# Kernel tuning notes

Hardware: AMD Instinct MI355X
Metric: run time of the kernel (lower is better)

Reference implementation:

```python
import jax, jax.numpy as jnp
import numpy as np

N_NODES = 100000
N_EDGES = 1600000
MUL = 32            # channel multiplicity for every irrep
INV_SQRT_MUL = 1.0 / np.sqrt(32.0)
# path constants: wigner-3j norms (1/sqrt3 for 0x1->1 and 1x1->0, 1/sqrt6 for 1x1->1)
# combined with fan-in path normalization (fan=32 for 0e out, fan=64 for 1o out, 2 paths)
C_DOT = 1.0 / np.sqrt(3.0 * 32.0)
C_SCL = 1.0 / np.sqrt(3.0 * 64.0)
C_CRS = 1.0 / np.sqrt(6.0 * 64.0)


def setup_inputs() -> dict:
    key = jax.random.key(0)
    ks = jax.random.split(key, 12)
    x = jax.random.normal(ks[0], (N_NODES, 128), jnp.float32)
    pos = jax.random.normal(ks[1], (N_NODES, 3), jnp.float32)
    edge_index = jax.random.randint(ks[2], (2, N_EDGES), 0, N_NODES, jnp.int32)
    # o3.Linear(32x0e+32x1o -> 32x0e+32x0e+32x1o): per-irrep channel mixing
    W_node_s = jax.random.normal(ks[3], (32, 64), jnp.float32)   # 0e -> (scalars|gates)
    W_node_v = jax.random.normal(ks[4], (32, 32), jnp.float32)   # 1o -> 1o
    # FullyConnectedTensorProduct(32x0e+32x1o, 1x1o -> 32x0e+32x1o): 3 CG paths
    W_tp_d = jax.random.normal(ks[5], (32, 32), jnp.float32)     # 1o x 1o -> 0e (dot)
    W_tp_s = jax.random.normal(ks[6], (32, 32), jnp.float32)     # 0e x 1o -> 1o
    W_tp_c = jax.random.normal(ks[7], (32, 32), jnp.float32)     # 1o x 1o -> 1o (cross)
    # o3.Linear(32x0e+32x1o -> 32x0e+32x1o)
    W_msg_s = jax.random.normal(ks[8], (32, 32), jnp.float32)
    W_msg_v = jax.random.normal(ks[9], (32, 32), jnp.float32)
    ln_gamma = jnp.ones((128,), jnp.float32)
    ln_beta = jnp.zeros((128,), jnp.float32)
    return {"x": x, "pos": pos, "edge_index": edge_index,
            "W_node_s": W_node_s, "W_node_v": W_node_v,
            "W_tp_d": W_tp_d, "W_tp_s": W_tp_s, "W_tp_c": W_tp_c,
            "W_msg_s": W_msg_s, "W_msg_v": W_msg_v,
            "ln_gamma": ln_gamma, "ln_beta": ln_beta}


def reference(x, pos, edge_index, W_node_s, W_node_v, W_tp_d, W_tp_s, W_tp_c,
              W_msg_s, W_msg_v, ln_gamma, ln_beta):
    N = x.shape[0]
    row, col = edge_index[0], edge_index[1]
    # split node irreps: 32 scalars (0e) | 32 vectors (1o) of dim 3
    s = x[:, :32]                       # [N,32]
    v = x[:, 32:].reshape(-1, 32, 3)    # [N,32,3]
    # lin_node (equivariant linear, path-normalized by 1/sqrt(fan_in)=1/sqrt(32))
    h_s = (s @ W_node_s) * INV_SQRT_MUL                          # [N,64]
    h_v = jnp.einsum('nid,ij->njd', v, W_node_v) * INV_SQRT_MUL  # [N,32,3]
    # Gate: relu scalars, sigmoid gates multiply the gated vectors
    sc = jax.nn.relu(h_s[:, :32])                                # [N,32]
    hv = h_v * jax.nn.sigmoid(h_s[:, 32:])[:, :, None]           # [N,32,3]
    # spherical harmonics l=1, component norm: sqrt(3)*unit vec in e3nn (y,z,x) order
    rel = pos[col] - pos[row]                                    # [E,3]
    unit = rel / jnp.sqrt(jnp.sum(rel * rel, -1, keepdims=True) + 1e-12)
    u = jnp.sqrt(3.0) * unit[:, (1, 2, 0)]                       # [E,3]
    # gather source-node features per edge
    sj = sc[col]                                                 # [E,32]
    vj = hv[col]                                                 # [E,32,3]
    # CG tensor product paths
    dot = jnp.einsum('eid,ed->ei', vj, u)                        # 1o x 1o -> 0e
    crs = jnp.cross(vj, u[:, None, :])                           # 1o x 1o -> 1o
    m0 = (dot @ W_tp_d) * C_DOT                                  # [E,32]
    m1 = (sj @ W_tp_s)[:, :, None] * u[:, None, :] * C_SCL \
         + jnp.einsum('eid,ik->ekd', crs, W_tp_c) * C_CRS        # [E,32,3]
    m = jnp.concatenate([m0, m1.reshape(-1, 96)], -1)            # [E,128]
    # scatter-mean over destination nodes (row)
    deg = jax.ops.segment_sum(jnp.ones_like(row, jnp.float32), row,
                              num_segments=N).clip(1.0)
    mi = jax.ops.segment_sum(m, row, num_segments=N) / deg[:, None]
    # lin_msg
    ms = (mi[:, :32] @ W_msg_s) * INV_SQRT_MUL
    mv = jnp.einsum('nid,ij->njd', mi[:, 32:].reshape(-1, 32, 3),
                    W_msg_v) * INV_SQRT_MUL
    o = jnp.concatenate([ms, mv.reshape(-1, 96)], -1)            # [N,128]
    # LayerNorm over 128 dims (as in the original, affine)
    mu = o.mean(-1, keepdims=True)
    var = o.var(-1, keepdims=True)
    o = (o - mu) / jnp.sqrt(var + 1e-5) * ln_gamma + ln_beta
    return x + o
```

## Files before the change

### kernel.cpp

```cpp
#include <hip/hip_runtime.h>
#include <math.h>


static constexpr float INV_SQRT_MUL = 0.17677669529663687f;
static constexpr float C_DOT = 0.10206207261596575f;
static constexpr float C_SCL = 0.07216878364870322f;
static constexpr float C_CRS = 0.05103103630798288f;
static constexpr float SQRT3 = 1.7320508075688772f;
static constexpr int MAXDEG = 48;
static constexpr int FEAT_B = 2048;
static constexpr int SCAT_B = 2048;

#define WS_ALIGN(x) (((x) + 255) & ~(size_t)255)

__device__ __forceinline__ unsigned short f2bf(float v) {
    unsigned int b = __float_as_uint(v);
    b += 0x7FFFu + ((b >> 16) & 1u);
    return (unsigned short)(b >> 16);
}
__device__ __forceinline__ float bf2f(unsigned short u) {
    return __uint_as_float(((unsigned int)u) << 16);
}

__global__ __launch_bounds__(1024)
void fuse_zero(const float* __restrict__ Wtpd, const float* __restrict__ Wtps,
               const float* __restrict__ Wtpc, const float* __restrict__ Wms,
               const float* __restrict__ Wmv, float* __restrict__ Wall,
               int* __restrict__ cnt, int N) {
    int t = threadIdx.x;
    if (blockIdx.x == 0) {
        int i = t >> 5, j = t & 31;
        float a = 0.f, b = 0.f, c = 0.f;
#pragma unroll
        for (int k = 0; k < 32; ++k) {
            a += Wtpd[i * 32 + k] * Wms[k * 32 + j];
            b += Wtps[i * 32 + k] * Wmv[k * 32 + j];
            c += Wtpc[i * 32 + k] * Wmv[k * 32 + j];
        }
        Wall[t]        = a * (C_DOT * INV_SQRT_MUL);
        Wall[1024 + t] = b * (C_SCL * INV_SQRT_MUL);
        Wall[2048 + t] = c * (C_CRS * INV_SQRT_MUL);
    } else {
        int i = (blockIdx.x - 1) * 1024 + t;
        if (i < N) cnt[i] = 0;
    }
}

template <bool FAT>
__global__ __launch_bounds__(128)
void phase1(const float* __restrict__ x, const float* __restrict__ Wns,
            const float* __restrict__ Wnv, const float* __restrict__ pos,
            const int* __restrict__ eidx, unsigned short* __restrict__ feat,
            int* __restrict__ cnt, void* __restrict__ slots_raw, int N, int E) {
    int t = threadIdx.x;
    if (blockIdx.x < FEAT_B) {
        float w[32], wg[32];
        int d = 0, pidx;
        if (t < 32) {
            pidx = t * 4;
#pragma unroll
            for (int k = 0; k < 32; ++k) w[k] = Wns[k * 64 + t];
        } else {
            int cc = t - 32; d = cc >> 5; int i = cc & 31;
            pidx = i * 4 + 1 + d;
#pragma unroll
            for (int k = 0; k < 32; ++k) { w[k] = Wnv[k * 32 + i]; wg[k] = Wns[k * 64 + 32 + i]; }
        }
        __shared__ float xs[128];
        for (int n = blockIdx.x; n < N; n += FEAT_B) {
            xs[t] = x[(size_t)n * 128 + t];
            __syncthreads();
            float val;
            if (t < 32) {
                float h = 0.f;
#pragma unroll
                for (int k = 0; k < 32; ++k) h += xs[k] * w[k];
                val = fmaxf(h * INV_SQRT_MUL, 0.f);
            } else {
                float h = 0.f, g = 0.f;
#pragma unroll
                for (int k = 0; k < 32; ++k) { h += xs[32 + k * 3 + d] * w[k]; g += xs[k] * wg[k]; }
                float sig = 1.f / (1.f + expf(-g * INV_SQRT_MUL));
                val = h * INV_SQRT_MUL * sig;
            }
            feat[(size_t)n * 128 + pidx] = f2bf(val);
            __syncthreads();
        }
    } else {
        int tid = (blockIdx.x - FEAT_B) * 128 + t;
        int Q = E >> 2;
        const int4* r4p = (const int4*)eidx;
        const int4* c4p = (const int4*)(eidx + E);
        float4* slotsF = (float4*)slots_raw;
        int*    slotsI = (int*)slots_raw;
        for (int q = tid; q < Q; q += SCAT_B * 128) {
            int4 R = r4p[q];
            int4 C = c4p[q];
            int rr[4] = {R.x, R.y, R.z, R.w};
            int cc[4] = {C.x, C.y, C.z, C.w};
            if (FAT) {
                float prx[4], pry[4], prz[4], pcx[4], pcy[4], pcz[4];
#pragma unroll
                for (int k = 0; k < 4; ++k) {
                    prx[k] = pos[rr[k] * 3 + 0]; pry[k] = pos[rr[k] * 3 + 1]; prz[k] = pos[rr[k] * 3 + 2];
                    pcx[k] = pos[cc[k] * 3 + 0]; pcy[k] = pos[cc[k] * 3 + 1]; pcz[k] = pos[cc[k] * 3 + 2];
                }
#pragma unroll
                for (int k = 0; k < 4; ++k) {
                    float rx = pcx[k] - prx[k], ry = pcy[k] - pry[k], rz = pcz[k] - prz[k];
                    float inv = rsqrtf(rx * rx + ry * ry + rz * rz + 1e-12f) * SQRT3;
                    int p = atomicAdd(&cnt[rr[k]], 1);
                    if (p < MAXDEG)
                        slotsF[(size_t)rr[k] * MAXDEG + p] =
                            make_float4(ry * inv, rz * inv, rx * inv, __int_as_float(cc[k]));
                }
            } else {
#pragma unroll
                for (int k = 0; k < 4; ++k) {
                    int p = atomicAdd(&cnt[rr[k]], 1);
                    if (p < MAXDEG) slotsI[(size_t)rr[k] * MAXDEG + p] = cc[k];
                }
            }
        }
        for (int e = (Q << 2) + tid; e < E; e += SCAT_B * 128) {
            int r = eidx[e], c = eidx[E + e];
            int p = atomicAdd(&cnt[r], 1);
            if (p < MAXDEG) {
                if (FAT) {
                    float rx = pos[c * 3 + 0] - pos[r * 3 + 0];
                    float ry = pos[c * 3 + 1] - pos[r * 3 + 1];
                    float rz = pos[c * 3 + 2] - pos[r * 3 + 2];
                    float inv = rsqrtf(rx * rx + ry * ry + rz * rz + 1e-12f) * SQRT3;
                    slotsF[(size_t)r * MAXDEG + p] = make_float4(ry * inv, rz * inv, rx * inv, __int_as_float(c));
                } else {
                    slotsI[(size_t)r * MAXDEG + p] = c;
                }
            }
        }
    }
}

__global__ __launch_bounds__(256)
void agg_fat(const float* __restrict__ x, const ushort4* __restrict__ feat,
             const int* __restrict__ cnt, const float4* __restrict__ slots,
             const float* __restrict__ Wall, const float* __restrict__ gamma,
             const float* __restrict__ beta, float* __restrict__ out, int N) {
    int t = threadIdx.x;
    __shared__ float wlds[3072];
    __shared__ float4 finA[8][32];
    __shared__ float4 finB[8][32];
    {
        float4* w4 = (float4*)wlds;
        const float4* g4 = (const float4*)Wall;
        for (int i = t; i < 768; i += 256) w4[i] = g4[i];
    }
    int hw = t >> 5, lane = t & 31;
    int n = blockIdx.x * 8 + hw;
    bool live = (n < N);
    int deg = live ? cnt[n] : 0;
    int c = min(deg, MAXDEG);
    const float4* bucket = slots + (size_t)(live ? n : 0) * MAXDEG;

    float D = 0.f, S0 = 0.f, S1 = 0.f, S2 = 0.f, C0 = 0.f, C1 = 0.f, C2 = 0.f;
    auto body = [&](int j) {
        float4 q = bucket[j];
        int col = __float_as_int(q.w);
        ushort4 f = feat[(size_t)col * 32 + lane];
        float sj = bf2f(f.x);
        float h0 = bf2f(f.y), h1 = bf2f(f.z), h2 = bf2f(f.w);
        D  += h0 * q.x + h1 * q.y + h2 * q.z;
        S0 += sj * q.x; S1 += sj * q.y; S2 += sj * q.z;
        C0 += h1 * q.z - h2 * q.y;
        C1 += h2 * q.x - h0 * q.z;
        C2 += h0 * q.y - h1 * q.x;
    };
    int j = 0;
    for (; j + 3 < c; j += 4) { body(j); body(j + 1); body(j + 2); body(j + 3); }
    for (; j < c; ++j) body(j);

    finA[hw][lane] = make_float4(D, S0, S1, S2);
    finB[hw][lane] = make_float4(C0, C1, C2, 0.f);
    __syncthreads();

    float invdeg = 1.0f / (float)((deg > 0) ? deg : 1);
    float a0 = 0.f, aV0 = 0.f, aV1 = 0.f, aV2 = 0.f;
#pragma unroll 8
    for (int i = 0; i < 32; ++i) {
        float4 a = finA[hw][i];
        float4 b = finB[hw][i];
        float wd = wlds[i * 32 + lane];
        float ws = wlds[1024 + i * 32 + lane];
        float wc = wlds[2048 + i * 32 + lane];
        a0  += a.x * wd;
        aV0 += a.y * ws + b.x * wc;
        aV1 += a.z * ws + b.y * wc;
        aV2 += a.w * ws + b.z * wc;
    }
    float vd = a0 * invdeg;
    float v0 = aV0 * invdeg, v1 = aV1 * invdeg, v2 = aV2 * invdeg;

    float s1 = vd + v0 + v1 + v2;
    float s2 = vd * vd + v0 * v0 + v1 * v1 + v2 * v2;
#pragma unroll
    for (int m = 16; m >= 1; m >>= 1) {
        s1 += __shfl_xor(s1, m);
        s2 += __shfl_xor(s2, m);
    }
    float mu = s1 * (1.f / 128.f);
    float var = s2 * (1.f / 128.f) - mu * mu;
    float rstd = rsqrtf(var + 1e-5f);

    if (live) {
        size_t base = (size_t)n * 128;
        int chv = 32 + lane * 3;
        float xv0 = __builtin_nontemporal_load(&x[base + lane]);
        float xa  = __builtin_nontemporal_load(&x[base + chv + 0]);
        float xb  = __builtin_nontemporal_load(&x[base + chv + 1]);
        float xc  = __builtin_nontemporal_load(&x[base + chv + 2]);
        __builtin_nontemporal_store(xv0 + (vd - mu) * rstd * gamma[lane] + beta[lane], &out[base + lane]);
        __builtin_nontemporal_store(xa + (v0 - mu) * rstd * gamma[chv + 0] + beta[chv + 0], &out[base + chv + 0]);
        __builtin_nontemporal_store(xb + (v1 - mu) * rstd * gamma[chv + 1] + beta[chv + 1], &out[base + chv + 1]);
        __builtin_nontemporal_store(xc + (v2 - mu) * rstd * gamma[chv + 2] + beta[chv + 2], &out[base + chv + 2]);
    }
}

__global__ __launch_bounds__(256)
void agg_thin(const float* __restrict__ x, const float* __restrict__ pos,
              const ushort4* __restrict__ feat, const int* __restrict__ cnt,
              const int* __restrict__ slots, const float* __restrict__ Wall,
              const float* __restrict__ gamma, const float* __restrict__ beta,
              float* __restrict__ out, int N) {
    int t = threadIdx.x;
    int hw = t >> 5, lane = t & 31;
    int n = blockIdx.x * 8 + hw;
    bool live = (n < N);

    __shared__ float4 cu[8][MAXDEG];
    __shared__ float4 finA[8][32];
    __shared__ float4 finB[8][32];

    int deg = live ? cnt[n] : 0;
    int c = min(deg, MAXDEG);

    float prx = 0.f, pry = 0.f, prz = 0.f;
    if (live) { prx = pos[n * 3 + 0]; pry = pos[n * 3 + 1]; prz = pos[n * 3 + 2]; }

    if (lane < c) {
        int col = slots[(size_t)n * MAXDEG + lane];
        float rx = pos[col * 3 + 0] - prx, ry = pos[col * 3 + 1] - pry, rz = pos[col * 3 + 2] - prz;
        float inv = rsqrtf(rx * rx + ry * ry + rz * rz + 1e-12f) * SQRT3;
        cu[hw][lane] = make_float4(ry * inv, rz * inv, rx * inv, __int_as_float(col));
    }
    if (c > 32 && lane < c - 32) {
        int col = slots[(size_t)n * MAXDEG + 32 + lane];
        float rx = pos[col * 3 + 0] - prx, ry = pos[col * 3 + 1] - pry, rz = pos[col * 3 + 2] - prz;
        float inv = rsqrtf(rx * rx + ry * ry + rz * rz + 1e-12f) * SQRT3;
        cu[hw][32 + lane] = make_float4(ry * inv, rz * inv, rx * inv, __int_as_float(col));
    }
    __syncthreads();

    float D = 0.f, S0 = 0.f, S1 = 0.f, S2 = 0.f, C0 = 0.f, C1 = 0.f, C2 = 0.f;
    for (int j = 0; j < c; ++j) {
        float4 q = cu[hw][j];
        int col = __float_as_int(q.w);
        ushort4 f = feat[(size_t)col * 32 + lane];
        float sj = bf2f(f.x);
        float h0 = bf2f(f.y), h1 = bf2f(f.z), h2 = bf2f(f.w);
        D  += h0 * q.x + h1 * q.y + h2 * q.z;
        S0 += sj * q.x; S1 += sj * q.y; S2 += sj * q.z;
        C0 += h1 * q.z - h2 * q.y;
        C1 += h2 * q.x - h0 * q.z;
        C2 += h0 * q.y - h1 * q.x;
    }
    finA[hw][lane] = make_float4(D, S0, S1, S2);
    finB[hw][lane] = make_float4(C0, C1, C2, 0.f);
    __syncthreads();

    float invdeg = 1.0f / (float)((deg > 0) ? deg : 1);
    float a0 = 0.f, aV0 = 0.f, aV1 = 0.f, aV2 = 0.f;
#pragma unroll 8
    for (int i = 0; i < 32; ++i) {
        float4 a = finA[hw][i];
        float4 b = finB[hw][i];
        float wd = Wall[i * 32 + lane];
        float ws = Wall[1024 + i * 32 + lane];
        float wc = Wall[2048 + i * 32 + lane];
        a0  += a.x * wd;
        aV0 += a.y * ws + b.x * wc;
        aV1 += a.z * ws + b.y * wc;
        aV2 += a.w * ws + b.z * wc;
    }
    float vd = a0 * invdeg;
    float v0 = aV0 * invdeg, v1 = aV1 * invdeg, v2 = aV2 * invdeg;

    float s1 = vd + v0 + v1 + v2;
    float s2 = vd * vd + v0 * v0 + v1 * v1 + v2 * v2;
#pragma unroll
    for (int m = 16; m >= 1; m >>= 1) {
        s1 += __shfl_xor(s1, m);
        s2 += __shfl_xor(s2, m);
    }
    float mu = s1 * (1.f / 128.f);
    float var = s2 * (1.f / 128.f) - mu * mu;
    float rstd = rsqrtf(var + 1e-5f);

    if (live) {
        size_t base = (size_t)n * 128;
        int chv = 32 + lane * 3;
        float xv0 = __builtin_nontemporal_load(&x[base + lane]);
        float xa  = __builtin_nontemporal_load(&x[base + chv + 0]);
        float xb  = __builtin_nontemporal_load(&x[base + chv + 1]);
        float xc  = __builtin_nontemporal_load(&x[base + chv + 2]);
        __builtin_nontemporal_store(xv0 + (vd - mu) * rstd * gamma[lane] + beta[lane], &out[base + lane]);
        __builtin_nontemporal_store(xa + (v0 - mu) * rstd * gamma[chv + 0] + beta[chv + 0], &out[base + chv + 0]);
        __builtin_nontemporal_store(xb + (v1 - mu) * rstd * gamma[chv + 1] + beta[chv + 1], &out[base + chv + 1]);
        __builtin_nontemporal_store(xc + (v2 - mu) * rstd * gamma[chv + 2] + beta[chv + 2], &out[base + chv + 2]);
    }
}

extern "C" void kernel_launch(void* const* d_in, const int* in_sizes, int n_in,
                              void* d_out, int out_size, void* d_ws, size_t ws_size,
                              hipStream_t stream) {
    const float* x     = (const float*)d_in[0];
    const float* pos   = (const float*)d_in[1];
    const int*   eidx  = (const int*)d_in[2];
    const float* Wns   = (const float*)d_in[3];
    const float* Wnv   = (const float*)d_in[4];
    const float* Wtpd  = (const float*)d_in[5];
    const float* Wtps  = (const float*)d_in[6];
    const float* Wtpc  = (const float*)d_in[7];
    const float* Wms   = (const float*)d_in[8];
    const float* Wmv   = (const float*)d_in[9];
    const float* gamma = (const float*)d_in[10];
    const float* beta  = (const float*)d_in[11];
    float* out = (float*)d_out;

    int N = in_sizes[0] / 128;
    int E = in_sizes[2] / 2;

    char* ws = (char*)d_ws;
    size_t off = 0;
    unsigned short* feat = (unsigned short*)(ws + off); off += WS_ALIGN((size_t)N * 128 * 2);
    int*   cnt  = (int*)(ws + off);   off += WS_ALIGN((size_t)N * 4);
    float* Wall = (float*)(ws + off); off += WS_ALIGN(3072 * 4);
    void*  slots = (void*)(ws + off);
    size_t fat_need = off + WS_ALIGN((size_t)N * MAXDEG * 16);
    bool fat = (fat_need <= ws_size);

    int zb = 1 + (N + 1023) / 1024;
    fuse_zero<<<zb, 1024, 0, stream>>>(Wtpd, Wtps, Wtpc, Wms, Wmv, Wall, cnt, N);
    if (fat) {
        phase1<true><<<FEAT_B + SCAT_B, 128, 0, stream>>>(x, Wns, Wnv, pos, eidx, feat, cnt, slots, N, E);
        agg_fat<<<(N + 7) / 8, 256, 0, stream>>>(x, (const ushort4*)feat, cnt, (const float4*)slots,
                                                 Wall, gamma, beta, out, N);
    } else {
        phase1<false><<<FEAT_B + SCAT_B, 128, 0, stream>>>(x, Wns, Wnv, pos, eidx, feat, cnt, slots, N, E);
        agg_thin<<<(N + 7) / 8, 256, 0, stream>>>(x, pos, (const ushort4*)feat, cnt, (const int*)slots,
                                                  Wall, gamma, beta, out, N);
    }
}
```

Before: 379.5 us.

## Bucket only column indices, compute edge geometry in aggregation, restructure node-feature phase

The scatter phase now stores just the int column index per bucket slot rather than a precomputed float4 unit vector, which cuts scatter traffic and the pos gathers done during scatter. The aggregation kernel gathers pos for each neighbor and recomputes the normalized edge vector, with 8-wide unrolled batches of independent loads. The node-feature phase is rewritten so each 64-lane wave handles one node, prefetches the next node's row, and writes packed ushort4 outputs. Block counts change to 1024+1024 blocks of 256 threads. The cost is extra pos gathers in the aggregation loop and the loss of the precomputed geometry path.

Result: slower. 478.4 us (+26.1%).

```diff
diff --git a/kernel.cpp b/kernel.cpp
--- a/kernel.cpp
+++ b/kernel.cpp
@@ -8,8 +8,8 @@
 static constexpr float C_CRS = 0.05103103630798288f;
 static constexpr float SQRT3 = 1.7320508075688772f;
 static constexpr int MAXDEG = 48;
-static constexpr int FEAT_B = 2048;
-static constexpr int SCAT_B = 2048;
+static constexpr int SCAT_B = 1024;
+static constexpr int FEAT_B = 1024;
 
 #define WS_ALIGN(x) (((x) + 255) & ~(size_t)255)
 
@@ -46,105 +46,143 @@
     }
 }
 
-template <bool FAT>
-__global__ __launch_bounds__(128)
+__global__ __launch_bounds__(256)
 void phase1(const float* __restrict__ x, const float* __restrict__ Wns,
-            const float* __restrict__ Wnv, const float* __restrict__ pos,
-            const int* __restrict__ eidx, unsigned short* __restrict__ feat,
-            int* __restrict__ cnt, void* __restrict__ slots_raw, int N, int E) {
+            const float* __restrict__ Wnv, const int* __restrict__ eidx,
+            ushort4* __restrict__ feat4, int* __restrict__ cnt,
+            int* __restrict__ slots, int N, int E) {
+    __shared__ float xs[4 * 128];
     int t = threadIdx.x;
-    if (blockIdx.x < FEAT_B) {
-        float w[32], wg[32];
-        int d = 0, pidx;
-        if (t < 32) {
-            pidx = t * 4;
-#pragma unroll
-            for (int k = 0; k < 32; ++k) w[k] = Wns[k * 64 + t];
-        } else {
-            int cc = t - 32; d = cc >> 5; int i = cc & 31;
-            pidx = i * 4 + 1 + d;
-#pragma unroll
-            for (int k = 0; k < 32; ++k) { w[k] = Wnv[k * 32 + i]; wg[k] = Wns[k * 64 + 32 + i]; }
-        }
-        __shared__ float xs[128];
-        for (int n = blockIdx.x; n < N; n += FEAT_B) {
-            xs[t] = x[(size_t)n * 128 + t];
-            __syncthreads();
-            float val;
-            if (t < 32) {
-                float h = 0.f;
-#pragma unroll
-                for (int k = 0; k < 32; ++k) h += xs[k] * w[k];
-                val = fmaxf(h * INV_SQRT_MUL, 0.f);
-            } else {
-                float h = 0.f, g = 0.f;
-#pragma unroll
-                for (int k = 0; k < 32; ++k) { h += xs[32 + k * 3 + d] * w[k]; g += xs[k] * wg[k]; }
-                float sig = 1.f / (1.f + expf(-g * INV_SQRT_MUL));
-                val = h * INV_SQRT_MUL * sig;
-            }
-            feat[(size_t)n * 128 + pidx] = f2bf(val);
-            __syncthreads();
-        }
-    } else {
-        int tid = (blockIdx.x - FEAT_B) * 128 + t;
+    if (blockIdx.x < SCAT_B) {
+        int tid = blockIdx.x * 256 + t;
         int Q = E >> 2;
         const int4* r4p = (const int4*)eidx;
         const int4* c4p = (const int4*)(eidx + E);
-        float4* slotsF = (float4*)slots_raw;
-        int*    slotsI = (int*)slots_raw;
-        for (int q = tid; q < Q; q += SCAT_B * 128) {
+        for (int q = tid; q < Q; q += SCAT_B * 256) {
             int4 R = r4p[q];
             int4 C = c4p[q];
             int rr[4] = {R.x, R.y, R.z, R.w};
             int cc[4] = {C.x, C.y, C.z, C.w};
-            if (FAT) {
-                float prx[4], pry[4], prz[4], pcx[4], pcy[4], pcz[4];
-#pragma unroll
-                for (int k = 0; k < 4; ++k) {
-                    prx[k] = pos[rr[k] * 3 + 0]; pry[k] = pos[rr[k] * 3 + 1]; prz[k] = pos[rr[k] * 3 + 2];
-                    pcx[k] = pos[cc[k] * 3 + 0]; pcy[k] = pos[cc[k] * 3 + 1]; pcz[k] = pos[cc[k] * 3 + 2];
-                }
-#pragma unroll
-                for (int k = 0; k < 4; ++k) {
-                    float rx = pcx[k] - prx[k], ry = pcy[k] - pry[k], rz = pcz[k] - prz[k];
-                    float inv = rsqrtf(rx * rx + ry * ry + rz * rz + 1e-12f) * SQRT3;
-                    int p = atomicAdd(&cnt[rr[k]], 1);
-                    if (p < MAXDEG)
-                        slotsF[(size_t)rr[k] * MAXDEG + p] =
-                            make_float4(ry * inv, rz * inv, rx * inv, __int_as_float(cc[k]));
-                }
-            } else {
-#pragma unroll
-                for (int k = 0; k < 4; ++k) {
-                    int p = atomicAdd(&cnt[rr[k]], 1);
-                    if (p < MAXDEG) slotsI[(size_t)rr[k] * MAXDEG + p] = cc[k];
-                }
-            }
-        }
-        for (int e = (Q << 2) + tid; e < E; e += SCAT_B * 128) {
+            int p[4];
+#pragma unroll
+            for (int k = 0; k < 4; ++k) p[k] = atomicAdd(&cnt[rr[k]], 1);
+#pragma unroll
+            for (int k = 0; k < 4; ++k)
+                if (p[k] < MAXDEG) slots[(size_t)rr[k] * MAXDEG + p[k]] = cc[k];
+        }
+        for (int e = (Q << 2) + tid; e < E; e += SCAT_B * 256) {
             int r = eidx[e], c = eidx[E + e];
             int p = atomicAdd(&cnt[r], 1);
-            if (p < MAXDEG) {
-                if (FAT) {
-                    float rx = pos[c * 3 + 0] - pos[r * 3 + 0];
-                    float ry = pos[c * 3 + 1] - pos[r * 3 + 1];
-                    float rz = pos[c * 3 + 2] - pos[r * 3 + 2];
-                    float inv = rsqrtf(rx * rx + ry * ry + rz * rz + 1e-12f) * SQRT3;
-                    slotsF[(size_t)r * MAXDEG + p] = make_float4(ry * inv, rz * inv, rx * inv, __int_as_float(c));
-                } else {
-                    slotsI[(size_t)r * MAXDEG + p] = c;
+            if (p < MAXDEG) slots[(size_t)r * MAXDEG + p] = c;
+        }
+    } else {
+        int wv = t >> 6, lane = t & 63;
+        int i = lane & 31;
+        float w[32], wg[32];
+        if (lane < 32) {
+#pragma unroll
+            for (int k = 0; k < 32; ++k) w[k] = Wns[k * 64 + i];
+        } else {
+#pragma unroll
+            for (int k = 0; k < 32; ++k) { w[k] = Wnv[k * 32 + i]; wg[k] = Wns[k * 64 + 32 + i]; }
+        }
+        float* xw = xs + wv * 128;
+        const float4* xw4 = (const float4*)xw;
+        const float2* x2 = (const float2*)x;
+        int wid = (blockIdx.x - SCAT_B) * 4 + wv;
+        const int stride = FEAT_B * 4;
+
+        int n = wid;
+        float2 cur = make_float2(0.f, 0.f);
+        if (n < N) cur = x2[(size_t)n * 64 + lane];
+        while (n < N) {
+            int n2 = n + stride;
+            float2 nxt = make_float2(0.f, 0.f);
+            if (n2 < N) nxt = x2[(size_t)n2 * 64 + lane];
+            ((float2*)xw)[lane] = cur;
+
+            float outS = 0.f, o0 = 0.f, o1 = 0.f, o2 = 0.f;
+            if (lane < 32) {
+                float h = 0.f;
+#pragma unroll
+                for (int j = 0; j < 8; ++j) {
+                    float4 q = xw4[j];
+                    h += q.x * w[4*j] + q.y * w[4*j+1] + q.z * w[4*j+2] + q.w * w[4*j+3];
                 }
+                outS = fmaxf(h * INV_SQRT_MUL, 0.f);
+            } else {
+                float gs = 0.f;
+#pragma unroll
+                for (int j = 0; j < 8; ++j) {
+                    float4 q = xw4[j];
+                    gs += q.x * wg[4*j] + q.y * wg[4*j+1] + q.z * wg[4*j+2] + q.w * wg[4*j+3];
+                }
+#pragma unroll
+                for (int j = 0; j < 24; ++j) {
+                    float4 q = xw4[8 + j];
+                    float vals[4] = {q.x, q.y, q.z, q.w};
+#pragma unroll
+                    for (int m = 0; m < 4; ++m) {
+                        int e = 4 * j + m;
+                        int k = e / 3, d = e % 3;
+                        float f = vals[m] * w[k];
+                        if (d == 0) o0 += f; else if (d == 1) o1 += f; else o2 += f;
+                    }
+                }
+                float sig = 1.f / (1.f + expf(-gs * INV_SQRT_MUL));
+                float sc = INV_SQRT_MUL * sig;
+                o0 *= sc; o1 *= sc; o2 *= sc;
             }
-        }
+            float scv = __shfl(outS, i);
+            if (lane >= 32) {
+                ushort4 pk;
+                pk.x = f2bf(scv); pk.y = f2bf(o0); pk.z = f2bf(o1); pk.w = f2bf(o2);
+                feat4[(size_t)n * 32 + i] = pk;
+            }
+            cur = nxt; n = n2;
+        }
+    }
+}
+
+template <int U>
+__device__ __forceinline__ void agg_chunk(const int* __restrict__ bucket, int j,
+    const ushort4* __restrict__ feat4, const float* __restrict__ pos,
+    int lane, float prx, float pry, float prz,
+    float& D, float& S0, float& S1, float& S2,
+    float& C0, float& C1, float& C2) {
+    int col[U];
+#pragma unroll
+    for (int k = 0; k < U; ++k) col[k] = bucket[j + k];
+    float px[U], py[U], pz[U];
+    ushort4 f[U];
+#pragma unroll
+    for (int k = 0; k < U; ++k) {
+        px[k] = pos[col[k] * 3 + 0];
+        py[k] = pos[col[k] * 3 + 1];
+        pz[k] = pos[col[k] * 3 + 2];
+        f[k]  = feat4[(size_t)col[k] * 32 + lane];
+    }
+#pragma unroll
+    for (int k = 0; k < U; ++k) {
+        float rx = px[k] - prx, ry = py[k] - pry, rz = pz[k] - prz;
+        float inv = rsqrtf(rx * rx + ry * ry + rz * rz + 1e-12f) * SQRT3;
+        float u0 = ry * inv, u1 = rz * inv, u2 = rx * inv;
+        float sj = bf2f(f[k].x);
+        float h0 = bf2f(f[k].y), h1 = bf2f(f[k].z), h2 = bf2f(f[k].w);
+        D  += h0 * u0 + h1 * u1 + h2 * u2;
+        S0 += sj * u0; S1 += sj * u1; S2 += sj * u2;
+        C0 += h1 * u2 - h2 * u1;
+        C1 += h2 * u0 - h0 * u2;
+        C2 += h0 * u1 - h1 * u0;
     }
 }
 
 __global__ __launch_bounds__(256)
-void agg_fat(const float* __restrict__ x, const ushort4* __restrict__ feat,
-             const int* __restrict__ cnt, const float4* __restrict__ slots,
-             const float* __restrict__ Wall, const float* __restrict__ gamma,
-             const float* __restrict__ beta, float* __restrict__ out, int N) {
+void agg(const float* __restrict__ x, const float* __restrict__ pos,
+         const ushort4* __restrict__ feat4, const int* __restrict__ cnt,
+         const int* __restrict__ slots, const float* __restrict__ Wall,
+         const float* __restrict__ gamma, const float* __restrict__ beta,
+         float* __restrict__ out, int N) {
     int t = threadIdx.x;
     __shared__ float wlds[3072];
     __shared__ float4 finA[8][32];
@@ -152,31 +190,27 @@
     {
         float4* w4 = (float4*)wlds;
         const float4* g4 = (const float4*)Wall;
-        for (int i = t; i < 768; i += 256) w4[i] = g4[i];
+        for (int i2 = t; i2 < 768; i2 += 256) w4[i2] = g4[i2];
     }
     int hw = t >> 5, lane = t & 31;
     int n = blockIdx.x * 8 + hw;
     bool live = (n < N);
+    int nn = live ? n : 0;
     int deg = live ? cnt[n] : 0;
     int c = min(deg, MAXDEG);
-    const float4* bucket = slots + (size_t)(live ? n : 0) * MAXDEG;
+    const int* bucket = slots + (size_t)nn * MAXDEG;
+    float prx = pos[nn * 3 + 0], pry = pos[nn * 3 + 1], prz = pos[nn * 3 + 2];
 
     float D = 0.f, S0 = 0.f, S1 = 0.f, S2 = 0.f, C0 = 0.f, C1 = 0.f, C2 = 0.f;
-    auto body = [&](int j) {
-        float4 q = bucket[j];
-        int col = __float_as_int(q.w);
-        ushort4 f = feat[(size_t)col * 32 + lane];
-        float sj = bf2f(f.x);
-        float h0 = bf2f(f.y), h1 = bf2f(f.z), h2 = bf2f(f.w);
-        D  += h0 * q.x + h1 * q.y + h2 * q.z;
-        S0 += sj * q.x; S1 += sj * q.y; S2 += sj * q.z;
-        C0 += h1 * q.z - h2 * q.y;
-        C1 += h2 * q.x - h0 * q.z;
-        C2 += h0 * q.y - h1 * q.x;
-    };
     int j = 0;
-    for (; j + 3 < c; j += 4) { body(j); body(j + 1); body(j + 2); body(j + 3); }
-    for (; j < c; ++j) body(j);
+    for (; j + 8 <= c; j += 8)
+        agg_chunk<8>(bucket, j, feat4, pos, lane, prx, pry, prz, D, S0, S1, S2, C0, C1, C2);
+    if (j + 4 <= c) {
+        agg_chunk<4>(bucket, j, feat4, pos, lane, prx, pry, prz, D, S0, S1, S2, C0, C1, C2);
+        j += 4;
+    }
+    for (; j < c; ++j)
+        agg_chunk<1>(bucket, j, feat4, pos, lane, prx, pry, prz, D, S0, S1, S2, C0, C1, C2);
 
     finA[hw][lane] = make_float4(D, S0, S1, S2);
     finB[hw][lane] = make_float4(C0, C1, C2, 0.f);
@@ -191,100 +225,6 @@
         float wd = wlds[i * 32 + lane];
         float ws = wlds[1024 + i * 32 + lane];
         float wc = wlds[2048 + i * 32 + lane];
-        a0  += a.x * wd;
-        aV0 += a.y * ws + b.x * wc;
-        aV1 += a.z * ws + b.y * wc;
-        aV2 += a.w * ws + b.z * wc;
-    }
-    float vd = a0 * invdeg;
-    float v0 = aV0 * invdeg, v1 = aV1 * invdeg, v2 = aV2 * invdeg;
-
-    float s1 = vd + v0 + v1 + v2;
-    float s2 = vd * vd + v0 * v0 + v1 * v1 + v2 * v2;
-#pragma unroll
-    for (int m = 16; m >= 1; m >>= 1) {
-        s1 += __shfl_xor(s1, m);
-        s2 += __shfl_xor(s2, m);
-    }
-    float mu = s1 * (1.f / 128.f);
-    float var = s2 * (1.f / 128.f) - mu * mu;
-    float rstd = rsqrtf(var + 1e-5f);
-
-    if (live) {
-        size_t base = (size_t)n * 128;
-        int chv = 32 + lane * 3;
-        float xv0 = __builtin_nontemporal_load(&x[base + lane]);
-        float xa  = __builtin_nontemporal_load(&x[base + chv + 0]);
-        float xb  = __builtin_nontemporal_load(&x[base + chv + 1]);
-        float xc  = __builtin_nontemporal_load(&x[base + chv + 2]);
-        __builtin_nontemporal_store(xv0 + (vd - mu) * rstd * gamma[lane] + beta[lane], &out[base + lane]);
-        __builtin_nontemporal_store(xa + (v0 - mu) * rstd * gamma[chv + 0] + beta[chv + 0], &out[base + chv + 0]);
-        __builtin_nontemporal_store(xb + (v1 - mu) * rstd * gamma[chv + 1] + beta[chv + 1], &out[base + chv + 1]);
-        __builtin_nontemporal_store(xc + (v2 - mu) * rstd * gamma[chv + 2] + beta[chv + 2], &out[base + chv + 2]);
-    }
-}
-
-__global__ __launch_bounds__(256)
-void agg_thin(const float* __restrict__ x, const float* __restrict__ pos,
-              const ushort4* __restrict__ feat, const int* __restrict__ cnt,
-              const int* __restrict__ slots, const float* __restrict__ Wall,
-              const float* __restrict__ gamma, const float* __restrict__ beta,
-              float* __restrict__ out, int N) {
-    int t = threadIdx.x;
-    int hw = t >> 5, lane = t & 31;
-    int n = blockIdx.x * 8 + hw;
-    bool live = (n < N);
-
-    __shared__ float4 cu[8][MAXDEG];
-    __shared__ float4 finA[8][32];
-    __shared__ float4 finB[8][32];
-
-    int deg = live ? cnt[n] : 0;
-    int c = min(deg, MAXDEG);
-
-    float prx = 0.f, pry = 0.f, prz = 0.f;
-    if (live) { prx = pos[n * 3 + 0]; pry = pos[n * 3 + 1]; prz = pos[n * 3 + 2]; }
-
-    if (lane < c) {
-        int col = slots[(size_t)n * MAXDEG + lane];
-        float rx = pos[col * 3 + 0] - prx, ry = pos[col * 3 + 1] - pry, rz = pos[col * 3 + 2] - prz;
-        float inv = rsqrtf(rx * rx + ry * ry + rz * rz + 1e-12f) * SQRT3;
-        cu[hw][lane] = make_float4(ry * inv, rz * inv, rx * inv, __int_as_float(col));
-    }
-    if (c > 32 && lane < c - 32) {
-        int col = slots[(size_t)n * MAXDEG + 32 + lane];
-        float rx = pos[col * 3 + 0] - prx, ry = pos[col * 3 + 1] - pry, rz = pos[col * 3 + 2] - prz;
-        float inv = rsqrtf(rx * rx + ry * ry + rz * rz + 1e-12f) * SQRT3;
-        cu[hw][32 + lane] = make_float4(ry * inv, rz * inv, rx * inv, __int_as_float(col));
-    }
-    __syncthreads();
-
-    float D = 0.f, S0 = 0.f, S1 = 0.f, S2 = 0.f, C0 = 0.f, C1 = 0.f, C2 = 0.f;
-    for (int j = 0; j < c; ++j) {
-        float4 q = cu[hw][j];
-        int col = __float_as_int(q.w);
-        ushort4 f = feat[(size_t)col * 32 + lane];
-        float sj = bf2f(f.x);
-        float h0 = bf2f(f.y), h1 = bf2f(f.z), h2 = bf2f(f.w);
-        D  += h0 * q.x + h1 * q.y + h2 * q.z;
-        S0 += sj * q.x; S1 += sj * q.y; S2 += sj * q.z;
-        C0 += h1 * q.z - h2 * q.y;
-        C1 += h2 * q.x - h0 * q.z;
-        C2 += h0 * q.y - h1 * q.x;
-    }
-    finA[hw][lane] = make_float4(D, S0, S1, S2);
-    finB[hw][lane] = make_float4(C0, C1, C2, 0.f);
-    __syncthreads();
-
-    float invdeg = 1.0f / (float)((deg > 0) ? deg : 1);
-    float a0 = 0.f, aV0 = 0.f, aV1 = 0.f, aV2 = 0.f;
-#pragma unroll 8
-    for (int i = 0; i < 32; ++i) {
-        float4 a = finA[hw][i];
-        float4 b = finB[hw][i];
-        float wd = Wall[i * 32 + lane];
-        float ws = Wall[1024 + i * 32 + lane];
-        float wc = Wall[2048 + i * 32 + lane];
         a0  += a.x * wd;
         aV0 += a.y * ws + b.x * wc;
         aV1 += a.z * ws + b.y * wc;
@@ -343,19 +283,10 @@
     unsigned short* feat = (unsigned short*)(ws + off); off += WS_ALIGN((size_t)N * 128 * 2);
     int*   cnt  = (int*)(ws + off);   off += WS_ALIGN((size_t)N * 4);
     float* Wall = (float*)(ws + off); off += WS_ALIGN(3072 * 4);
-    void*  slots = (void*)(ws + off);
-    size_t fat_need = off + WS_ALIGN((size_t)N * MAXDEG * 16);
-    bool fat = (fat_need <= ws_size);
+    int*   slots = (int*)(ws + off);
 
     int zb = 1 + (N + 1023) / 1024;
     fuse_zero<<<zb, 1024, 0, stream>>>(Wtpd, Wtps, Wtpc, Wms, Wmv, Wall, cnt, N);
-    if (fat) {
-        phase1<true><<<FEAT_B + SCAT_B, 128, 0, stream>>>(x, Wns, Wnv, pos, eidx, feat, cnt, slots, N, E);
-        agg_fat<<<(N + 7) / 8, 256, 0, stream>>>(x, (const ushort4*)feat, cnt, (const float4*)slots,
-                                                 Wall, gamma, beta, out, N);
-    } else {
-        phase1<false><<<FEAT_B + SCAT_B, 128, 0, stream>>>(x, Wns, Wnv, pos, eidx, feat, cnt, slots, N, E);
-        agg_thin<<<(N + 7) / 8, 256, 0, stream>>>(x, pos, (const ushort4*)feat, cnt, (const int*)slots,
-                                                  Wall, gamma, beta, out, N);
-    }
-}
+    phase1<<<SCAT_B + FEAT_B, 256, 0, stream>>>(x, Wns, Wnv, eidx, (ushort4*)feat, cnt, slots, N, E);
+    agg<<<(N + 7) / 8, 256, 0, stream>>>(x, pos, (const ushort4*)feat, cnt, slots, Wall, gamma, beta, out, N);
+}
```
